# Kernel optimization log

Hardware: AMD Instinct MI355X
Metric: run time of the kernel (lower is better)

## Reference

```python
import jax, jax.numpy as jnp
import numpy as np

N_NODES = 100000  # m == n for the square adjacency
LEAKY_SLOPE = 0.5


def setup_inputs() -> dict:
    key = jax.random.key(0)
    k1, k2, k3 = jax.random.split(key, 3)
    E = 3200000
    D = 128
    edge_index = jax.random.randint(k1, (2, E), 0, N_NODES, dtype=jnp.int64)
    edge_vals = jax.random.uniform(k2, (E,), dtype=jnp.float32)
    embeds = jax.random.normal(k3, (N_NODES, D), dtype=jnp.float32)
    return {"edge_index": edge_index, "edge_vals": edge_vals, "embeds": embeds}


def reference(edge_index, edge_vals, embeds):
    # coalesce (sum duplicate (row,col) values) followed by scatter-add SpMM
    # is equivalent to scatter-add SpMM directly on un-coalesced indices.
    row, col = edge_index[0], edge_index[1]
    # gather source embeddings, scale by edge values, segment-sum into rows
    msgs = edge_vals[:, None] * embeds[col]                 # [E, D]
    agg = jax.ops.segment_sum(msgs, row, num_segments=N_NODES)  # [N, D]
    return jax.nn.leaky_relu(agg, negative_slope=LEAKY_SLOPE)
```

## Files before the change

kernel.cpp:

```cpp
#include <hip/hip_runtime.h>
#include <hip/hip_fp16.h>


#define GCN_D       128
#define LEAKY_SLOPE 0.5f
#define NBLK        256
#define RPB         16
#define RPB_SH      4
#define RWV         2
#define CAP         1024
#define NBINS_MAX   8192
#define NCHAIN_FB   4

typedef int      i32x4 __attribute__((ext_vector_type(4)));
typedef float    f32x2 __attribute__((ext_vector_type(2)));
typedef float    f32x4 __attribute__((ext_vector_type(4)));
typedef unsigned u32x2 __attribute__((ext_vector_type(2)));
typedef unsigned u32x4 __attribute__((ext_vector_type(4)));

__device__ inline unsigned pack_half2(float a, float b) {
    __half2 h = __floats2half2_rn(a, b);
    return *reinterpret_cast<unsigned*>(&h);
}

__device__ inline f32x2 h2_to_f2(__half2 h) {
    float2 f = __half22float2(h);
    f32x2 r; r.x = f.x; r.y = f.y;
    return r;
}


__global__ void hist_convert_kernel(const int* __restrict__ row,
                                    int E, int CH, int nbins,
                                    unsigned* __restrict__ histT,
                                    const f32x4* __restrict__ emb4,
                                    int n8,
                                    u32x4* __restrict__ h8) {
    __shared__ unsigned h[NBINS_MAX];
    if ((int)blockIdx.x < NBLK) {
        int b = blockIdx.x;
        for (int i = threadIdx.x; i < nbins; i += blockDim.x) h[i] = 0u;
        __syncthreads();
        int s = b * CH;
        int e = min(E, s + CH);
        int n = e - s;
        int g4 = n >> 2;
        const i32x4* row4 = reinterpret_cast<const i32x4*>(row + s);
        for (int g = threadIdx.x; g < g4; g += blockDim.x) {
            i32x4 r4 = row4[g];
            atomicAdd(&h[r4.x >> RPB_SH], 1u);
            atomicAdd(&h[r4.y >> RPB_SH], 1u);
            atomicAdd(&h[r4.z >> RPB_SH], 1u);
            atomicAdd(&h[r4.w >> RPB_SH], 1u);
        }
        for (int i = s + (g4 << 2) + threadIdx.x; i < e; i += blockDim.x)
            atomicAdd(&h[row[i] >> RPB_SH], 1u);
        __syncthreads();
        for (int i = threadIdx.x; i < nbins; i += blockDim.x)
            histT[(long long)b * nbins + i] = h[i];
    } else {
        int bid = (int)blockIdx.x - NBLK;
        int nb  = (int)gridDim.x - NBLK;
        int stride = nb * blockDim.x;
        for (int i = bid * blockDim.x + threadIdx.x; i < n8; i += stride) {
            f32x4 a  = __builtin_nontemporal_load(&emb4[2 * i]);
            f32x4 b2 = __builtin_nontemporal_load(&emb4[2 * i + 1]);
            u32x4 o;
            o.x = pack_half2(a.x, a.y);
            o.y = pack_half2(a.z, a.w);
            o.z = pack_half2(b2.x, b2.y);
            o.w = pack_half2(b2.z, b2.w);
            h8[i] = o;
        }
    }
}


__global__ void __launch_bounds__(256)
scanT_kernel(unsigned* __restrict__ histT, int nbins,
             unsigned* __restrict__ tot) {
    int bin = blockIdx.x * 256 + threadIdx.x;
    if (bin >= nbins) return;
    unsigned run = 0;
    for (int blk = 0; blk < NBLK; blk += 8) {
        unsigned v[8];
        #pragma unroll
        for (int k = 0; k < 8; ++k)
            v[k] = histT[(long long)(blk + k) * nbins + bin];
        #pragma unroll
        for (int k = 0; k < 8; ++k) {
            unsigned t = v[k];
            histT[(long long)(blk + k) * nbins + bin] = run;
            run += t;
        }
    }
    tot[bin] = run;
}


__global__ void __launch_bounds__(1024)
scanBase_kernel(const unsigned* __restrict__ tot, int nbins,
                unsigned* __restrict__ base, int E) {
    __shared__ unsigned part[1024];
    int t = threadIdx.x;
    int chunk = (nbins + 1023) >> 10;
    long long s = (long long)t * chunk;

    unsigned acc = 0;
    for (int i = 0; i < chunk; ++i) {
        long long j = s + i;
        if (j < nbins) acc += tot[j];
    }
    part[t] = acc;
    __syncthreads();
    for (int off = 1; off < 1024; off <<= 1) {
        unsigned v = (t >= off) ? part[t - off] : 0u;
        __syncthreads();
        part[t] += v;
        __syncthreads();
    }
    unsigned run = (t == 0) ? 0u : part[t - 1];
    for (int i = 0; i < chunk; ++i) {
        long long j = s + i;
        if (j < nbins) {
            unsigned v = tot[j];
            base[j] = run;
            run += v;
        }
    }
    if (t == 1023) base[nbins] = (unsigned)E;
}


__global__ void __launch_bounds__(1024)
scatter_kernel(const int* __restrict__ row,
               const int* __restrict__ col,
               const float* __restrict__ val,
               int E, int CH, int nbins,
               const unsigned* __restrict__ histT,
               const unsigned* __restrict__ base,
               u32x2* __restrict__ entry) {
    __shared__ unsigned cur[NBINS_MAX];
    int b = blockIdx.x;
    for (int i = threadIdx.x; i < nbins; i += blockDim.x)
        cur[i] = histT[(long long)b * nbins + i] + base[i];
    __syncthreads();

    int s = b * CH;
    int e = min(E, s + CH);
    int n = e - s;
    int g4 = n >> 2;

    const i32x4* row4 = reinterpret_cast<const i32x4*>(row + s);
    const i32x4* col4 = reinterpret_cast<const i32x4*>(col + s);
    const f32x4* val4 = reinterpret_cast<const f32x4*>(val + s);

    for (int g = threadIdx.x; g < g4; g += 1024) {
        i32x4 r4 = row4[g];
        i32x4 c4 = col4[g];
        f32x4 v4 = val4[g];
        #pragma unroll
        for (int k = 0; k < 4; ++k) {
            int r = r4[k];
            unsigned key = ((unsigned)(r & (RPB - 1)) << 17) | (unsigned)c4[k];
            unsigned pos = atomicAdd(&cur[r >> RPB_SH], 1u);
            u32x2 q; q.x = key; q.y = __float_as_uint(v4[k]);
            entry[pos] = q;
        }
    }
    for (int i = s + (g4 << 2) + threadIdx.x; i < e; i += 1024) {
        int r = row[i];
        unsigned key = ((unsigned)(r & (RPB - 1)) << 17) | (unsigned)col[i];
        unsigned pos = atomicAdd(&cur[r >> RPB_SH], 1u);
        u32x2 q; q.x = key; q.y = __float_as_uint(val[i]);
        entry[pos] = q;
    }
}


__global__ void __launch_bounds__(512)
bin_reduce_kernel(const unsigned* __restrict__ base,
                  const u32x2* __restrict__ entry,
                  const __half2* __restrict__ ebh,
                  float* __restrict__ out,
                  int E, int N, int nbins) {
    __shared__ u32x2    sorted[CAP];
    __shared__ unsigned cnt[64];
    __shared__ unsigned offs[64];
    __shared__ unsigned cur[64];

    int b    = blockIdx.x;
    int tid  = threadIdx.x;
    int wave = tid >> 6;
    int lane = tid & 63;

    int seg0 = (int)base[b];
    int seg1 = (int)base[b + 1];

    f32x2 acc[RWV];
    #pragma unroll
    for (int j = 0; j < RWV; ++j) { acc[j].x = 0.f; acc[j].y = 0.f; }

    for (int cs = seg0; cs < seg1; cs += CAP) {
        int n = min(CAP, seg1 - cs);

        if (tid < 64) cnt[tid] = 0u;
        __syncthreads();

        for (int i = tid; i < n; i += 512) {
            u32x2 q = entry[cs + i];
            atomicAdd(&cnt[q.x >> 17], 1u);
        }
        __syncthreads();

        if (wave == 0) {
            unsigned c = cnt[lane];
            unsigned s = c;
            #pragma unroll
            for (int off = 1; off < 64; off <<= 1) {
                unsigned t = __shfl_up(s, off, 64);
                if (lane >= off) s += t;
            }
            offs[lane] = s - c;
            cur[lane]  = s - c;
        }
        __syncthreads();

        for (int i = tid; i < n; i += 512) {
            u32x2 q = entry[cs + i];
            unsigned pos = atomicAdd(&cur[q.x >> 17], 1u);
            sorted[pos] = q;
        }
        __syncthreads();

        #pragma unroll
        for (int j = 0; j < RWV; ++j) {
            int r  = wave * RWV + j;
            int s  = (int)offs[r];
            int en = s + (int)cnt[r];
            int i  = s;
            for (; i + 8 <= en; i += 8) {
                u32x2 q0 = sorted[i],     q1 = sorted[i + 1];
                u32x2 q2 = sorted[i + 2], q3 = sorted[i + 3];
                u32x2 q4 = sorted[i + 4], q5 = sorted[i + 5];
                u32x2 q6 = sorted[i + 6], q7 = sorted[i + 7];
                __half2 m0 = ebh[(long long)(q0.x & 0x1FFFFu) * 64 + lane];
                __half2 m1 = ebh[(long long)(q1.x & 0x1FFFFu) * 64 + lane];
                __half2 m2 = ebh[(long long)(q2.x & 0x1FFFFu) * 64 + lane];
                __half2 m3 = ebh[(long long)(q3.x & 0x1FFFFu) * 64 + lane];
                __half2 m4 = ebh[(long long)(q4.x & 0x1FFFFu) * 64 + lane];
                __half2 m5 = ebh[(long long)(q5.x & 0x1FFFFu) * 64 + lane];
                __half2 m6 = ebh[(long long)(q6.x & 0x1FFFFu) * 64 + lane];
                __half2 m7 = ebh[(long long)(q7.x & 0x1FFFFu) * 64 + lane];
                f32x2 vv;
                vv.x = vv.y = __uint_as_float(q0.y); acc[j] += vv * h2_to_f2(m0);
                vv.x = vv.y = __uint_as_float(q1.y); acc[j] += vv * h2_to_f2(m1);
                vv.x = vv.y = __uint_as_float(q2.y); acc[j] += vv * h2_to_f2(m2);
                vv.x = vv.y = __uint_as_float(q3.y); acc[j] += vv * h2_to_f2(m3);
                vv.x = vv.y = __uint_as_float(q4.y); acc[j] += vv * h2_to_f2(m4);
                vv.x = vv.y = __uint_as_float(q5.y); acc[j] += vv * h2_to_f2(m5);
                vv.x = vv.y = __uint_as_float(q6.y); acc[j] += vv * h2_to_f2(m6);
                vv.x = vv.y = __uint_as_float(q7.y); acc[j] += vv * h2_to_f2(m7);
            }
            if (i + 4 <= en) {
                u32x2 q0 = sorted[i],     q1 = sorted[i + 1];
                u32x2 q2 = sorted[i + 2], q3 = sorted[i + 3];
                __half2 m0 = ebh[(long long)(q0.x & 0x1FFFFu) * 64 + lane];
                __half2 m1 = ebh[(long long)(q1.x & 0x1FFFFu) * 64 + lane];
                __half2 m2 = ebh[(long long)(q2.x & 0x1FFFFu) * 64 + lane];
                __half2 m3 = ebh[(long long)(q3.x & 0x1FFFFu) * 64 + lane];
                f32x2 vv;
                vv.x = vv.y = __uint_as_float(q0.y); acc[j] += vv * h2_to_f2(m0);
                vv.x = vv.y = __uint_as_float(q1.y); acc[j] += vv * h2_to_f2(m1);
                vv.x = vv.y = __uint_as_float(q2.y); acc[j] += vv * h2_to_f2(m2);
                vv.x = vv.y = __uint_as_float(q3.y); acc[j] += vv * h2_to_f2(m3);
                i += 4;
            }
            for (; i < en; ++i) {
                u32x2 qq = sorted[i];
                __half2 mm = ebh[(long long)(qq.x & 0x1FFFFu) * 64 + lane];
                f32x2 vv; vv.x = vv.y = __uint_as_float(qq.y);
                acc[j] += vv * h2_to_f2(mm);
            }
        }
        __syncthreads();
    }

    int gr0 = b * RPB + wave * RWV;
    #pragma unroll
    for (int j = 0; j < RWV; ++j) {
        int gr = gr0 + j;
        if (gr < N) {
            float x = acc[j].x, y = acc[j].y;
            x = x > 0.f ? x : LEAKY_SLOPE * x;
            y = y > 0.f ? y : LEAKY_SLOPE * y;
            f32x2 o; o.x = x; o.y = y;
            __builtin_nontemporal_store(
                o, reinterpret_cast<f32x2*>(out) + (long long)gr * 64 + lane);
        }
    }
}


__global__ void build_nodes_kernel(const int* __restrict__ row,
                                   const int* __restrict__ col,
                                   const float* __restrict__ val,
                                   int E,
                                   int* __restrict__ head,
                                   int4* __restrict__ node) {
    int stride = gridDim.x * blockDim.x;
    for (int i = blockIdx.x * blockDim.x + threadIdx.x; i < E; i += stride) {
        int   r = row[i];
        int   c = col[i];
        float v = val[i];
        int prev = atomicExch(&head[r * NCHAIN_FB + (i & (NCHAIN_FB - 1))], i);
        node[i] = make_int4(prev, c, __float_as_int(v), 0);
    }
}

__global__ void __launch_bounds__(256)
reduce_nodes_kernel(const int* __restrict__ head,
                    const int4* __restrict__ node,
                    const float* __restrict__ embeds,
                    float* __restrict__ out,
                    int N) {
    int wave = (int)((blockIdx.x * (long long)blockDim.x + threadIdx.x) >> 6);
    int lane = threadIdx.x & 63;
    if (wave >= N) return;

    const float2* eb = reinterpret_cast<const float2*>(embeds);
    int4 h = reinterpret_cast<const int4*>(head)[wave];
    int e0 = h.x, e1 = h.y, e2 = h.z, e3 = h.w;

    float ax = 0.f, ay = 0.f;

    while ((e0 & e1 & e2 & e3) != -1) {
        int i0 = e0 >= 0 ? e0 : 0;
        int i1 = e1 >= 0 ? e1 : 0;
        int i2 = e2 >= 0 ? e2 : 0;
        int i3 = e3 >= 0 ? e3 : 0;

        int4 n0 = node[i0];
        int4 n1 = node[i1];
        int4 n2 = node[i2];
        int4 n3 = node[i3];

        int c0 = e0 >= 0 ? n0.y : 0;
        int c1 = e1 >= 0 ? n1.y : 0;
        int c2 = e2 >= 0 ? n2.y : 0;
        int c3 = e3 >= 0 ? n3.y : 0;

        float2 m0 = eb[(long long)c0 * 64 + lane];
        float2 m1 = eb[(long long)c1 * 64 + lane];
        float2 m2 = eb[(long long)c2 * 64 + lane];
        float2 m3 = eb[(long long)c3 * 64 + lane];

        float v0 = e0 >= 0 ? __int_as_float(n0.z) : 0.f;
        float v1 = e1 >= 0 ? __int_as_float(n1.z) : 0.f;
        float v2 = e2 >= 0 ? __int_as_float(n2.z) : 0.f;
        float v3 = e3 >= 0 ? __int_as_float(n3.z) : 0.f;

        ax += v0 * m0.x; ay += v0 * m0.y;
        ax += v1 * m1.x; ay += v1 * m1.y;
        ax += v2 * m2.x; ay += v2 * m2.y;
        ax += v3 * m3.x; ay += v3 * m3.y;

        e0 = e0 >= 0 ? n0.x : -1;
        e1 = e1 >= 0 ? n1.x : -1;
        e2 = e2 >= 0 ? n2.x : -1;
        e3 = e3 >= 0 ? n3.x : -1;
    }

    ax = ax > 0.f ? ax : LEAKY_SLOPE * ax;
    ay = ay > 0.f ? ay : LEAKY_SLOPE * ay;
    reinterpret_cast<float2*>(out)[(long long)wave * 64 + lane] =
        make_float2(ax, ay);
}


__global__ void gcn_scatter_kernel(const int* __restrict__ row_idx,
                                   const int* __restrict__ col_idx,
                                   const float* __restrict__ vals,
                                   const float* __restrict__ embeds,
                                   float* __restrict__ out,
                                   int E) {
    long long tid = (long long)blockIdx.x * blockDim.x + threadIdx.x;
    long long e = tid >> 5;
    if (e >= E) return;
    int q = (int)(tid & 31);
    int row = row_idx[e];
    int col = col_idx[e];
    float v = vals[e];
    const float4* src =
        reinterpret_cast<const float4*>(embeds + (long long)col * GCN_D) + q;
    float4 m = *src;
    float* dst = out + (long long)row * GCN_D + (long long)q * 4;
    atomicAdd(dst + 0, v * m.x);
    atomicAdd(dst + 1, v * m.y);
    atomicAdd(dst + 2, v * m.z);
    atomicAdd(dst + 3, v * m.w);
}

__global__ void gcn_leaky_relu_kernel(float* __restrict__ out, int n4) {
    int i = blockIdx.x * blockDim.x + threadIdx.x;
    if (i >= n4) return;
    float4* p = reinterpret_cast<float4*>(out) + i;
    float4 x = *p;
    x.x = x.x > 0.f ? x.x : LEAKY_SLOPE * x.x;
    x.y = x.y > 0.f ? x.y : LEAKY_SLOPE * x.y;
    x.z = x.z > 0.f ? x.z : LEAKY_SLOPE * x.z;
    x.w = x.w > 0.f ? x.w : LEAKY_SLOPE * x.w;
    *p = x;
}


extern "C" void kernel_launch(void* const* d_in, const int* in_sizes, int n_in,
                              void* d_out, int out_size, void* d_ws, size_t ws_size,
                              hipStream_t stream) {
    const int*   edge_index = (const int*)d_in[0];
    const float* edge_vals  = (const float*)d_in[1];
    const float* embeds     = (const float*)d_in[2];
    float*       out        = (float*)d_out;

    const int E = in_sizes[1];
    const int N = out_size / GCN_D;
    const int* row = edge_index;
    const int* col = edge_index + E;

    const int block = 256;
    const int nbins = (N + RPB - 1) / RPB;
    const int M     = NBLK * nbins;
    const int CH    = (E + NBLK - 1) / NBLK;

    size_t hist_b = (((size_t)M * sizeof(unsigned)) + 255) & ~(size_t)255;
    size_t tot_b  = (((size_t)nbins * sizeof(unsigned)) + 255) & ~(size_t)255;
    size_t base_b = (((size_t)(nbins + 1) * sizeof(unsigned)) + 255) & ~(size_t)255;
    size_t ent_b  = (((size_t)E * sizeof(u32x2)) + 255) & ~(size_t)255;
    size_t half_b = (size_t)N * GCN_D * sizeof(__half);
    size_t need_r15 = hist_b + tot_b + base_b + ent_b + half_b;

    size_t head_fb = (size_t)N * NCHAIN_FB * sizeof(int);
    size_t need_r3 = head_fb + (size_t)E * sizeof(int4);

    if (ws_size >= need_r15 && nbins <= NBINS_MAX) {
        char* p = (char*)d_ws;
        unsigned* histT = (unsigned*)p;                 p += hist_b;
        unsigned* tot   = (unsigned*)p;                 p += tot_b;
        unsigned* base  = (unsigned*)p;                 p += base_b;
        u32x2*    entry = reinterpret_cast<u32x2*>(p);  p += ent_b;
        u32x4*    h8    = reinterpret_cast<u32x4*>(p);

        int n8 = N * (GCN_D / 8);
        int convBlocks = (n8 + block - 1) / block;

        hist_convert_kernel<<<NBLK + convBlocks, block, 0, stream>>>(
            row, E, CH, nbins, histT,
            reinterpret_cast<const f32x4*>(embeds), n8, h8);

        scanT_kernel<<<(nbins + 255) / 256, 256, 0, stream>>>(histT, nbins, tot);
        scanBase_kernel<<<1, 1024, 0, stream>>>(tot, nbins, base, E);

        scatter_kernel<<<NBLK, 1024, 0, stream>>>(
            row, col, edge_vals, E, CH, nbins, histT, base, entry);

        bin_reduce_kernel<<<nbins, 512, 0, stream>>>(
            base, entry, reinterpret_cast<const __half2*>(h8), out, E, N, nbins);
    } else if (ws_size >= need_r3) {
        int*  head = (int*)d_ws;
        int4* node = reinterpret_cast<int4*>((char*)d_ws + head_fb);

        hipMemsetAsync(head, 0xFF, head_fb, stream);
        build_nodes_kernel<<<2048, block, 0, stream>>>(row, col, edge_vals,
                                                       E, head, node);

        long long threads = (long long)N * 64;
        int rblocks = (int)((threads + block - 1) / block);
        reduce_nodes_kernel<<<rblocks, block, 0, stream>>>(
            head, node, embeds, out, N);
    } else {
        hipMemsetAsync(d_out, 0, (size_t)out_size * sizeof(float), stream);
        long long total_threads = (long long)E * 32;
        long long grid = (total_threads + block - 1) / block;
        gcn_scatter_kernel<<<(unsigned)grid, block, 0, stream>>>(
            row, col, edge_vals, embeds, out, E);
        int n4 = out_size / 4;
        gcn_leaky_relu_kernel<<<(n4 + 255) / 256, 256, 0, stream>>>(out, n4);
    }
}
```

Before: 193.3 us.

## Parallelize column histogram scan into segmented passes and single-pass bin sort

The per-bin exclusive scan over 256 block histograms, previously a serial loop in only about 25 blocks, is split into three kernels: segment partial sums across a 2D grid, a short scan over 16 segment sums, and a parallel write-back of offsets. Separately, the in-block counting sort in bin_reduce keeps the atomicAdd return value as the rank, so entries are read from global once and the second atomic pass and cur array go away. This adds two kernel launches and a psum workspace buffer in exchange for more parallelism in the scan phase and fewer global reads and atomics in the reduce phase.

```diff
diff --git a/kernel.cpp b/kernel.cpp
--- a/kernel.cpp
+++ b/kernel.cpp
@@ -9,6 +9,8 @@
 #define RPB_SH      4
 #define RWV         2
 #define CAP         1024
+#define SEG         16
+#define SEGROWS     16
 #define NBINS_MAX   8192
 #define NCHAIN_FB   4
 
@@ -77,22 +79,33 @@
 
 
 __global__ void __launch_bounds__(256)
-scanT_kernel(unsigned* __restrict__ histT, int nbins,
-             unsigned* __restrict__ tot) {
+scanT1_kernel(const unsigned* __restrict__ histT, int nbins,
+              unsigned* __restrict__ psum) {
+    int bin = blockIdx.x * 256 + threadIdx.x;
+    int seg = blockIdx.y;
+    if (bin >= nbins) return;
+    const unsigned* p = histT + (long long)seg * SEGROWS * nbins + bin;
+    unsigned v[SEGROWS];
+    #pragma unroll
+    for (int k = 0; k < SEGROWS; ++k) v[k] = p[(long long)k * nbins];
+    unsigned s = 0;
+    #pragma unroll
+    for (int k = 0; k < SEGROWS; ++k) s += v[k];
+    psum[(long long)seg * nbins + bin] = s;
+}
+
+
+__global__ void __launch_bounds__(256)
+scanT2_kernel(unsigned* __restrict__ psum, int nbins,
+              unsigned* __restrict__ tot) {
     int bin = blockIdx.x * 256 + threadIdx.x;
     if (bin >= nbins) return;
     unsigned run = 0;
-    for (int blk = 0; blk < NBLK; blk += 8) {
-        unsigned v[8];
-        #pragma unroll
-        for (int k = 0; k < 8; ++k)
-            v[k] = histT[(long long)(blk + k) * nbins + bin];
-        #pragma unroll
-        for (int k = 0; k < 8; ++k) {
-            unsigned t = v[k];
-            histT[(long long)(blk + k) * nbins + bin] = run;
-            run += t;
-        }
+    #pragma unroll
+    for (int seg = 0; seg < SEG; ++seg) {
+        unsigned t = psum[(long long)seg * nbins + bin];
+        psum[(long long)seg * nbins + bin] = run;
+        run += t;
     }
     tot[bin] = run;
 }
@@ -129,6 +142,25 @@
         }
     }
     if (t == 1023) base[nbins] = (unsigned)E;
+}
+
+
+__global__ void __launch_bounds__(256)
+scanT3_kernel(unsigned* __restrict__ histT, int nbins,
+              const unsigned* __restrict__ psum) {
+    int bin = blockIdx.x * 256 + threadIdx.x;
+    int seg = blockIdx.y;
+    if (bin >= nbins) return;
+    unsigned run = psum[(long long)seg * nbins + bin];
+    unsigned* p = histT + (long long)seg * SEGROWS * nbins + bin;
+    unsigned v[SEGROWS];
+    #pragma unroll
+    for (int k = 0; k < SEGROWS; ++k) v[k] = p[(long long)k * nbins];
+    #pragma unroll
+    for (int k = 0; k < SEGROWS; ++k) {
+        p[(long long)k * nbins] = run;
+        run += v[k];
+    }
 }
 
 
@@ -187,7 +219,6 @@
     __shared__ u32x2    sorted[CAP];
     __shared__ unsigned cnt[64];
     __shared__ unsigned offs[64];
-    __shared__ unsigned cur[64];
 
     int b    = blockIdx.x;
     int tid  = threadIdx.x;
@@ -207,9 +238,16 @@
         if (tid < 64) cnt[tid] = 0u;
         __syncthreads();
 
-        for (int i = tid; i < n; i += 512) {
-            u32x2 q = entry[cs + i];
-            atomicAdd(&cnt[q.x >> 17], 1u);
+        u32x2 q0, q1;
+        unsigned r0 = 0, r1 = 0;
+        bool h0 = tid < n, h1 = tid + 512 < n;
+        if (h0) {
+            q0 = entry[cs + tid];
+            r0 = atomicAdd(&cnt[q0.x >> 17], 1u);
+        }
+        if (h1) {
+            q1 = entry[cs + tid + 512];
+            r1 = atomicAdd(&cnt[q1.x >> 17], 1u);
         }
         __syncthreads();
 
@@ -222,15 +260,11 @@
                 if (lane >= off) s += t;
             }
             offs[lane] = s - c;
-            cur[lane]  = s - c;
-        }
-        __syncthreads();
-
-        for (int i = tid; i < n; i += 512) {
-            u32x2 q = entry[cs + i];
-            unsigned pos = atomicAdd(&cur[q.x >> 17], 1u);
-            sorted[pos] = q;
-        }
+        }
+        __syncthreads();
+
+        if (h0) sorted[offs[q0.x >> 17] + r0] = q0;
+        if (h1) sorted[offs[q1.x >> 17] + r1] = q1;
         __syncthreads();
 
         #pragma unroll
@@ -240,40 +274,40 @@
             int en = s + (int)cnt[r];
             int i  = s;
             for (; i + 8 <= en; i += 8) {
-                u32x2 q0 = sorted[i],     q1 = sorted[i + 1];
-                u32x2 q2 = sorted[i + 2], q3 = sorted[i + 3];
-                u32x2 q4 = sorted[i + 4], q5 = sorted[i + 5];
-                u32x2 q6 = sorted[i + 6], q7 = sorted[i + 7];
-                __half2 m0 = ebh[(long long)(q0.x & 0x1FFFFu) * 64 + lane];
-                __half2 m1 = ebh[(long long)(q1.x & 0x1FFFFu) * 64 + lane];
-                __half2 m2 = ebh[(long long)(q2.x & 0x1FFFFu) * 64 + lane];
-                __half2 m3 = ebh[(long long)(q3.x & 0x1FFFFu) * 64 + lane];
-                __half2 m4 = ebh[(long long)(q4.x & 0x1FFFFu) * 64 + lane];
-                __half2 m5 = ebh[(long long)(q5.x & 0x1FFFFu) * 64 + lane];
-                __half2 m6 = ebh[(long long)(q6.x & 0x1FFFFu) * 64 + lane];
-                __half2 m7 = ebh[(long long)(q7.x & 0x1FFFFu) * 64 + lane];
+                u32x2 e0 = sorted[i],     e1 = sorted[i + 1];
+                u32x2 e2 = sorted[i + 2], e3 = sorted[i + 3];
+                u32x2 e4 = sorted[i + 4], e5 = sorted[i + 5];
+                u32x2 e6 = sorted[i + 6], e7 = sorted[i + 7];
+                __half2 m0 = ebh[(long long)(e0.x & 0x1FFFFu) * 64 + lane];
+                __half2 m1 = ebh[(long long)(e1.x & 0x1FFFFu) * 64 + lane];
+                __half2 m2 = ebh[(long long)(e2.x & 0x1FFFFu) * 64 + lane];
+                __half2 m3 = ebh[(long long)(e3.x & 0x1FFFFu) * 64 + lane];
+                __half2 m4 = ebh[(long long)(e4.x & 0x1FFFFu) * 64 + lane];
+                __half2 m5 = ebh[(long long)(e5.x & 0x1FFFFu) * 64 + lane];
+                __half2 m6 = ebh[(long long)(e6.x & 0x1FFFFu) * 64 + lane];
+                __half2 m7 = ebh[(long long)(e7.x & 0x1FFFFu) * 64 + lane];
                 f32x2 vv;
-                vv.x = vv.y = __uint_as_float(q0.y); acc[j] += vv * h2_to_f2(m0);
-                vv.x = vv.y = __uint_as_float(q1.y); acc[j] += vv * h2_to_f2(m1);
-                vv.x = vv.y = __uint_as_float(q2.y); acc[j] += vv * h2_to_f2(m2);
-                vv.x = vv.y = __uint_as_float(q3.y); acc[j] += vv * h2_to_f2(m3);
-                vv.x = vv.y = __uint_as_float(q4.y); acc[j] += vv * h2_to_f2(m4);
-                vv.x = vv.y = __uint_as_float(q5.y); acc[j] += vv * h2_to_f2(m5);
-                vv.x = vv.y = __uint_as_float(q6.y); acc[j] += vv * h2_to_f2(m6);
-                vv.x = vv.y = __uint_as_float(q7.y); acc[j] += vv * h2_to_f2(m7);
+                vv.x = vv.y = __uint_as_float(e0.y); acc[j] += vv * h2_to_f2(m0);
+                vv.x = vv.y = __uint_as_float(e1.y); acc[j] += vv * h2_to_f2(m1);
+                vv.x = vv.y = __uint_as_float(e2.y); acc[j] += vv * h2_to_f2(m2);
+                vv.x = vv.y = __uint_as_float(e3.y); acc[j] += vv * h2_to_f2(m3);
+                vv.x = vv.y = __uint_as_float(e4.y); acc[j] += vv * h2_to_f2(m4);
+                vv.x = vv.y = __uint_as_float(e5.y); acc[j] += vv * h2_to_f2(m5);
+                vv.x = vv.y = __uint_as_float(e6.y); acc[j] += vv * h2_to_f2(m6);
+                vv.x = vv.y = __uint_as_float(e7.y); acc[j] += vv * h2_to_f2(m7);
             }
             if (i + 4 <= en) {
-                u32x2 q0 = sorted[i],     q1 = sorted[i + 1];
-                u32x2 q2 = sorted[i + 2], q3 = sorted[i + 3];
-                __half2 m0 = ebh[(long long)(q0.x & 0x1FFFFu) * 64 + lane];
-                __half2 m1 = ebh[(long long)(q1.x & 0x1FFFFu) * 64 + lane];
-                __half2 m2 = ebh[(long long)(q2.x & 0x1FFFFu) * 64 + lane];
-                __half2 m3 = ebh[(long long)(q3.x & 0x1FFFFu) * 64 + lane];
+                u32x2 e0 = sorted[i],     e1 = sorted[i + 1];
+                u32x2 e2 = sorted[i + 2], e3 = sorted[i + 3];
+                __half2 m0 = ebh[(long long)(e0.x & 0x1FFFFu) * 64 + lane];
+                __half2 m1 = ebh[(long long)(e1.x & 0x1FFFFu) * 64 + lane];
+                __half2 m2 = ebh[(long long)(e2.x & 0x1FFFFu) * 64 + lane];
+                __half2 m3 = ebh[(long long)(e3.x & 0x1FFFFu) * 64 + lane];
                 f32x2 vv;
-                vv.x = vv.y = __uint_as_float(q0.y); acc[j] += vv * h2_to_f2(m0);
-                vv.x = vv.y = __uint_as_float(q1.y); acc[j] += vv * h2_to_f2(m1);
-                vv.x = vv.y = __uint_as_float(q2.y); acc[j] += vv * h2_to_f2(m2);
-                vv.x = vv.y = __uint_as_float(q3.y); acc[j] += vv * h2_to_f2(m3);
+                vv.x = vv.y = __uint_as_float(e0.y); acc[j] += vv * h2_to_f2(m0);
+                vv.x = vv.y = __uint_as_float(e1.y); acc[j] += vv * h2_to_f2(m1);
+                vv.x = vv.y = __uint_as_float(e2.y); acc[j] += vv * h2_to_f2(m2);
+                vv.x = vv.y = __uint_as_float(e3.y); acc[j] += vv * h2_to_f2(m3);
                 i += 4;
             }
             for (; i < en; ++i) {
@@ -433,18 +467,20 @@
     const int CH    = (E + NBLK - 1) / NBLK;
 
     size_t hist_b = (((size_t)M * sizeof(unsigned)) + 255) & ~(size_t)255;
+    size_t psum_b = (((size_t)SEG * nbins * sizeof(unsigned)) + 255) & ~(size_t)255;
     size_t tot_b  = (((size_t)nbins * sizeof(unsigned)) + 255) & ~(size_t)255;
     size_t base_b = (((size_t)(nbins + 1) * sizeof(unsigned)) + 255) & ~(size_t)255;
     size_t ent_b  = (((size_t)E * sizeof(u32x2)) + 255) & ~(size_t)255;
     size_t half_b = (size_t)N * GCN_D * sizeof(__half);
-    size_t need_r15 = hist_b + tot_b + base_b + ent_b + half_b;
+    size_t need_r16 = hist_b + psum_b + tot_b + base_b + ent_b + half_b;
 
     size_t head_fb = (size_t)N * NCHAIN_FB * sizeof(int);
     size_t need_r3 = head_fb + (size_t)E * sizeof(int4);
 
-    if (ws_size >= need_r15 && nbins <= NBINS_MAX) {
+    if (ws_size >= need_r16 && nbins <= NBINS_MAX) {
         char* p = (char*)d_ws;
         unsigned* histT = (unsigned*)p;                 p += hist_b;
+        unsigned* psum  = (unsigned*)p;                 p += psum_b;
         unsigned* tot   = (unsigned*)p;                 p += tot_b;
         unsigned* base  = (unsigned*)p;                 p += base_b;
         u32x2*    entry = reinterpret_cast<u32x2*>(p);  p += ent_b;
@@ -457,8 +493,11 @@
             row, E, CH, nbins, histT,
             reinterpret_cast<const f32x4*>(embeds), n8, h8);
 
-        scanT_kernel<<<(nbins + 255) / 256, 256, 0, stream>>>(histT, nbins, tot);
+        dim3 segGrid((nbins + 255) / 256, SEG);
+        scanT1_kernel<<<segGrid, 256, 0, stream>>>(histT, nbins, psum);
+        scanT2_kernel<<<(nbins + 255) / 256, 256, 0, stream>>>(psum, nbins, tot);
         scanBase_kernel<<<1, 1024, 0, stream>>>(tot, nbins, base, E);
+        scanT3_kernel<<<segGrid, 256, 0, stream>>>(histT, nbins, psum);
 
         scatter_kernel<<<NBLK, 1024, 0, stream>>>(
             row, col, edge_vals, E, CH, nbins, histT, base, entry);
```

Measured after the change: 190.1 us. No clear change (-1.7%).
